# Kernel tuning notes

Measured on AMD Instinct MI355X. Metric: run time of the kernel, lower is better.

Reference implementation:

```python
import jax, jax.numpy as jnp
import numpy as np

N = 100000   # node_count
F = 128      # dim_in (also top-k pool size: k = ceil(F/N * N) = F)
E = 625000   # edges


def setup_inputs() -> dict:
    key = jax.random.key(0)
    ks = jax.random.split(key, 20)
    s = 1.0 / np.sqrt(F)

    def g(i, shape, scale=s):
        return jax.random.normal(ks[i], shape, dtype=jnp.float32) * scale

    inp = {
        "x": jax.random.normal(ks[0], (N, F), dtype=jnp.float32),
        "edge_index": jax.random.randint(ks[1], (2, E), 0, N),
        "edge_weight": jax.random.uniform(ks[2], (E,), dtype=jnp.float32),
    }
    for l in (1, 2):
        b = 3 + 6 * (l - 1)
        inp[f"p{l}"] = g(b, (F,))              # TopKPooling projection vector
        inp[f"w_ih{l}"] = g(b + 1, (3 * F, F))  # GRU input weights (r,z,n)
        inp[f"w_hh{l}"] = g(b + 2, (3 * F, F))  # GRU hidden weights
        inp[f"b_ih{l}"] = g(b + 3, (3 * F,))
        inp[f"b_hh{l}"] = g(b + 4, (3 * F,))
        inp[f"h0{l}"] = g(b + 5, (F, F))        # EvolveGCNH initial_weight
    inp["lin1_w"] = g(15, (2, F))
    inp["lin1_b"] = g(16, (2,), 0.1)
    inp["lin2_w"] = g(17, (1, 2), 0.5)
    inp["lin2_b"] = g(18, (1,), 0.1)
    return inp


def _gru_step(x_t, h, w_ih, w_hh, b_ih, b_hh):
    # single GRU timestep, batch = F rows, hidden = F
    gi = x_t @ w_ih.T + b_ih
    gh = h @ w_hh.T + b_hh
    i_r, i_z, i_n = jnp.split(gi, 3, axis=-1)
    h_r, h_z, h_n = jnp.split(gh, 3, axis=-1)
    r = jax.nn.sigmoid(i_r + h_r)
    z = jax.nn.sigmoid(i_z + h_z)
    n = jnp.tanh(i_n + r * h_n)
    return (1.0 - z) * n + z * h


def _gcn_conv_fixed_w(x, W, edge_index, edge_weight):
    # GCN with externally supplied weight: out = D^-1/2 (A+I) D^-1/2 (x W)
    row, col = edge_index[0], edge_index[1]
    loops = jnp.arange(N)
    row = jnp.concatenate([row, loops])
    col = jnp.concatenate([col, loops])
    w = jnp.concatenate([edge_weight, jnp.ones((N,), x.dtype)])
    deg = jax.ops.segment_sum(w, col, num_segments=N)
    dinv = jnp.where(deg > 0, jax.lax.rsqrt(deg), 0.0)
    norm = dinv[row] * w * dinv[col]          # [E+N]
    xw = x @ W                                 # [N, F]
    return jax.ops.segment_sum(norm[:, None] * xw[row], col, num_segments=N)


def _evolve_gcnh(x, edge_index, edge_weight, p, w_ih, w_hh, b_ih, b_hh, h0):
    # TopKPooling: score = x@p / ||p||, keep top F nodes, gate by tanh(score)
    score = x @ p / jnp.linalg.norm(p)
    top_vals, top_idx = jax.lax.top_k(score, F)
    x_tilde = x[top_idx] * jnp.tanh(top_vals)[:, None]   # [F, F]
    # evolve weight via one GRU step (hidden = previous/initial weight)
    W = _gru_step(x_tilde, h0, w_ih, w_hh, b_ih, b_hh)   # [F, F]
    return _gcn_conv_fixed_w(x, W, edge_index, edge_weight)


def reference(x, edge_index, edge_weight,
              p1, w_ih1, w_hh1, b_ih1, b_hh1, h01,
              p2, w_ih2, w_hh2, b_ih2, b_hh2, h02,
              lin1_w, lin1_b, lin2_w, lin2_b):
    h = jax.nn.relu(_evolve_gcnh(x, edge_index, edge_weight, p1, w_ih1, w_hh1, b_ih1, b_hh1, h01))
    h = jax.nn.relu(_evolve_gcnh(h, edge_index, edge_weight, p2, w_ih2, w_hh2, b_ih2, b_hh2, h02))
    # dropout(0.4) is identity in eval mode
    h = h @ lin1_w.T + lin1_b
    h = h @ lin2_w.T + lin2_b
    return h  # [N, 1]
```

## Files before the change

### kernel.cpp

```cpp
#include <hip/hip_runtime.h>
#include <cstdint>
#include <cstddef>


#define FDIM 128

typedef __attribute__((ext_vector_type(8))) short bfrag;
typedef __attribute__((ext_vector_type(4))) float f32x4;
typedef __attribute__((ext_vector_type(2))) float f32x2;

__device__ __forceinline__ float wave_sum(float v) {
#pragma unroll
  for (int m = 32; m >= 1; m >>= 1) v += __shfl_xor(v, m, 64);
  return v;
}

__device__ __forceinline__ float sigmoidf_(float x) {
  return 1.0f / (1.0f + expf(-x));
}

__device__ __forceinline__ unsigned omap(float f) {
  unsigned u = __float_as_uint(f);
  return (u & 0x80000000u) ? ~u : (u | 0x80000000u);
}

__device__ __forceinline__ int xcd_chunk(int b, int nb) {
  return (b & 7) * (nb >> 3) + (b >> 3);
}

__device__ __forceinline__ int swz(int row, int colb) {
  return row * 256 + (colb ^ ((row & 7) << 4));
}


__global__ void k_edge_deg(const int* __restrict__ ei, const float* __restrict__ ew,
                           float* deg, int* cnt, int E) {
  int e = blockIdx.x * blockDim.x + threadIdx.x;
  if (e < E) {
    int c = ei[E + e];
    atomicAdd(&deg[c], ew[e]);
    atomicAdd(&cnt[c], 1);
  }
}

__global__ void k_scan1(const int* __restrict__ cnt, int* bsum,
                        const float* __restrict__ deg, float* __restrict__ dinv, int n) {
  __shared__ int s[256];
  int b = blockIdx.x, t = threadIdx.x;
  int base = b * 1024;
  int v = 0;
#pragma unroll
  for (int j = 0; j < 4; j++) {
    int i = base + j * 256 + t;
    if (i < n) { v += cnt[i]; dinv[i] = 1.0f / sqrtf(1.0f + deg[i]); }
  }
  s[t] = v; __syncthreads();
  for (int off = 128; off > 0; off >>= 1) { if (t < off) s[t] += s[t + off]; __syncthreads(); }
  if (t == 0) bsum[b] = s[0];
}

__global__ __launch_bounds__(128) void k_scan2_setup(
    int* bsum, int nb, int* rstartN,
    const float* p1, const float* p2, float* invn1, float* invn2,
    const float* l1w, const float* l1b, const float* l2w, const float* l2b,
    float* v, float* cc) {
  __shared__ int s[1024];
  int t = threadIdx.x;
  for (int i = t; i < nb; i += 128) s[i] = bsum[i];
  __syncthreads();
  if (t == 0) {
    int run = 0;
    for (int b = 0; b < nb; b++) { int x = s[b]; s[b] = run; run += x; }
    s[1023] = run;
  }
  __syncthreads();
  for (int i = t; i < nb; i += 128) bsum[i] = s[i];
  if (t == 0) rstartN[0] = s[1023];
  int wv = t >> 6, l = t & 63;
  const float* p = wv ? p2 : p1;
  float2 pv = ((const float2*)p)[l];
  float ss = wave_sum(pv.x * pv.x + pv.y * pv.y);
  if (l == 0) (wv ? invn2 : invn1)[0] = 1.0f / sqrtf(ss);
  v[t] = l2w[0] * l1w[t] + l2w[1] * l1w[128 + t];
  if (t == 0) cc[0] = l2w[0] * l1b[0] + l2w[1] * l1b[1] + l2b[0];
}

__global__ __launch_bounds__(1024) void k_scan3(const int* __restrict__ cnt,
                                                const int* __restrict__ bsum,
                                                int* rstart, int* rnext, int n) {
  __shared__ int s[1024];
  int b = blockIdx.x, t = threadIdx.x;
  int i = b * 1024 + t;
  int v = (i < n) ? cnt[i] : 0;
  s[t] = v; __syncthreads();
  for (int off = 1; off < 1024; off <<= 1) {
    int tmp = (t >= off) ? s[t - off] : 0;
    __syncthreads();
    s[t] += tmp;
    __syncthreads();
  }
  if (i < n) { int ex = bsum[b] + s[t] - v; rstart[i] = ex; rnext[i] = ex; }
}

__global__ void k_fill(const int* __restrict__ ei, const float* __restrict__ ew,
                       const float* __restrict__ dinv, int* rnext, int2* pay, int E) {
  int e = blockIdx.x * blockDim.x + threadIdx.x;
  if (e < E) {
    int r = ei[e];
    int c = ei[E + e];
    float nm = dinv[r] * ew[e] * dinv[c];
    int pos = atomicAdd(&rnext[c], 1);
    pay[pos] = make_int2(r, __float_as_int(nm));
  }
}


__global__ void k_sampdots(const float* __restrict__ x, const float* __restrict__ p,
                           const float* __restrict__ invn, float* __restrict__ samp,
                           int stride) {
  int l = threadIdx.x & 63;
  int w = blockIdx.x * 4 + (threadIdx.x >> 6);
  float2 pv = ((const float2*)p)[l];
  float inv = invn[0];
#pragma unroll
  for (int r = 0; r < 4; r++) {
    int si = w * 4 + r;
    float2 a = ((const float2*)(x + (size_t)(si * stride) * FDIM))[l];
    float s = wave_sum(a.x * pv.x + a.y * pv.y) * inv;
    if (l == 0) samp[si] = s;
  }
}

template <int STRIDED>
__global__ __launch_bounds__(256) void k_thr16(const float* __restrict__ src, int stride,
                                               float* __restrict__ thr) {
  __shared__ float a[2048];
  int t = threadIdx.x;
  for (int i = t; i < 2048; i += 256)
    a[i] = STRIDED ? src[(size_t)i * stride] : src[i];
  __syncthreads();
  int g = blockIdx.x * 256 + t;
  int j = g >> 2, sub = g & 3;
  float v = a[j];
  int gt = 0, eq = 0;
  const float4* a4 = (const float4*)(a + sub * 512);
#pragma unroll 8
  for (int i = 0; i < 128; i++) {
    float4 b = a4[i];
    gt += (b.x > v) + (b.y > v) + (b.z > v) + (b.w > v);
    eq += (b.x == v) + (b.y == v) + (b.z == v) + (b.w == v);
  }
  gt += __shfl_xor(gt, 1, 64); eq += __shfl_xor(eq, 1, 64);
  gt += __shfl_xor(gt, 2, 64); eq += __shfl_xor(eq, 2, 64);
  if (sub == 0 && gt <= 15 && gt + eq > 15) thr[0] = v;
}

__global__ void k_collect(const float* __restrict__ sc, const float* __restrict__ thr,
                          unsigned long long* candk, int* csel, int n) {
  int i = blockIdx.x * blockDim.x + threadIdx.x;
  if (i >= n) return;
  float s = sc[i];
  if (s >= thr[0]) {
    int pos = atomicAdd(csel, 1);
    if (pos < 4096)
      candk[pos] = ((unsigned long long)omap(s) << 32) | (unsigned)(~(unsigned)i);
  }
}

__global__ __launch_bounds__(1024) void k_sel(const unsigned long long* __restrict__ candk,
                                              const int* __restrict__ csel,
                                              int* tidx, float* ttanh) {
  __shared__ unsigned long long a[4104];
  int t = threadIdx.x;
  int nc = csel[0]; if (nc > 4096) nc = 4096;
  int ncp = (nc + 7) & ~7;
  for (int i = t; i < ncp; i += 1024) a[i] = (i < nc) ? candk[i] : 0ULL;
  __syncthreads();
  for (int j = t; j < nc; j += 1024) {
    unsigned long long key = a[j];
    int r = 0;
#pragma unroll 8
    for (int i = 0; i < ncp; i++) r += (a[i] > key);
    if (r < 128) {
      unsigned idx = ~(unsigned)key;
      unsigned hi = (unsigned)(key >> 32);
      unsigned u = (hi & 0x80000000u) ? (hi ^ 0x80000000u) : ~hi;
      tidx[r] = (int)idx;
      ttanh[r] = tanhf(__uint_as_float(u));
    }
  }
}


template <int BF16IN>
__global__ __launch_bounds__(384) void k_gru(const void* __restrict__ xinv,
                                             const int* __restrict__ tidx,
                                             const float* __restrict__ ttanh,
                                             const float* __restrict__ wih,
                                             const float* __restrict__ whh,
                                             const float* __restrict__ bih,
                                             const float* __restrict__ bhh,
                                             const float* __restrict__ h0,
                                             unsigned short* __restrict__ WT_hi,
                                             unsigned short* __restrict__ WT_lo) {
  __shared__ float xt[128], hs[128], gis[384], ghs[384];
  int r = blockIdx.x, t = threadIdx.x;
  if (t < 128) {
    int idx = tidx[r];
    float xv;
    if (BF16IN) {
      unsigned short u = ((const unsigned short*)xinv)[(size_t)idx * FDIM + t];
      xv = __uint_as_float((unsigned)u << 16);
    } else {
      xv = ((const float*)xinv)[(size_t)idx * FDIM + t];
    }
    xt[t] = xv * ttanh[r];
    hs[t] = h0[r * FDIM + t];
  }
  __syncthreads();
  float gi = bih[t], gh = bhh[t];
  const float4* wi4 = (const float4*)(wih + (size_t)t * FDIM);
  const float4* wh4 = (const float4*)(whh + (size_t)t * FDIM);
#pragma unroll 8
  for (int k = 0; k < 32; k++) {
    float4 av = wi4[k], bv = wh4[k];
    gi += av.x * xt[4 * k] + av.y * xt[4 * k + 1] + av.z * xt[4 * k + 2] + av.w * xt[4 * k + 3];
    gh += bv.x * hs[4 * k] + bv.y * hs[4 * k + 1] + bv.z * hs[4 * k + 2] + bv.w * hs[4 * k + 3];
  }
  gis[t] = gi; ghs[t] = gh;
  __syncthreads();
  if (t < 128) {
    float rg = sigmoidf_(gis[t] + ghs[t]);
    float zg = sigmoidf_(gis[t + 128] + ghs[t + 128]);
    float ng = tanhf(gis[t + 256] + rg * ghs[t + 256]);
    float w = (1.0f - zg) * ng + zg * hs[t];
    unsigned u = __float_as_uint(w);
    float res = w - __uint_as_float(u & 0xFFFF0000u);
    WT_hi[t * FDIM + r] = (unsigned short)(u >> 16);
    WT_lo[t * FDIM + r] = (unsigned short)(__float_as_uint(res) >> 16);
  }
}


template <int MODE>
__global__ __launch_bounds__(256) void k_gemm5(const float* __restrict__ Af,
                                               const unsigned short* __restrict__ Ab,
                                               const unsigned short* __restrict__ BTh,
                                               const unsigned short* __restrict__ BTl,
                                               unsigned short* __restrict__ Y2,
                                               float* __restrict__ scOut,
                                               const float* __restrict__ pvec,
                                               const float* __restrict__ invn2,
                                               const float* __restrict__ cc,
                                               int nrows) {
  __shared__ unsigned short sBh[128 * 128];
  __shared__ unsigned short sBl[128 * 128];
  int tid = threadIdx.x;
  int eb = xcd_chunk(blockIdx.x, gridDim.x);
  int rblk = eb * 128;
  if (rblk >= nrows) return;
  for (int i = tid; i < 2048; i += 256) {
    int row = i >> 4, colb = (i & 15) << 4;
    *(uint4*)((char*)sBh + swz(row, colb)) = ((const uint4*)BTh)[i];
    *(uint4*)((char*)sBl + swz(row, colb)) = ((const uint4*)BTl)[i];
  }
  __syncthreads();
  int wv = tid >> 6, l = tid & 63;
  int lcol = l & 15;
  int kgrp = (l >> 4) * 8;

  float pv[8];
#pragma unroll
  for (int ct = 0; ct < 8; ct++) pv[ct] = pvec[ct * 16 + lcol];
  float scale = (MODE == 1) ? invn2[0] : cc[0];

  for (int tile = 0; tile < 2; tile++) {
    int r0 = rblk + wv * 32 + tile * 16;
    if (r0 >= nrows) break;
    int arow = min(r0 + lcol, nrows - 1);
    f32x4 acc[8];
#pragma unroll
    for (int c = 0; c < 8; c++) acc[c] = (f32x4){0.f, 0.f, 0.f, 0.f};
#pragma unroll
    for (int ks = 0; ks < 4; ks++) {
      bfrag ah, al;
      if (MODE == 1) {
        const float* xp = Af + (size_t)arow * FDIM + kgrp + ks * 32;
        float4 v0 = *(const float4*)(xp);
        float4 v1 = *(const float4*)(xp + 4);
        float xs[8] = {v0.x, v0.y, v0.z, v0.w, v1.x, v1.y, v1.z, v1.w};
#pragma unroll
        for (int i = 0; i < 8; i++) {
          unsigned u = __float_as_uint(xs[i]);
          float res = xs[i] - __uint_as_float(u & 0xFFFF0000u);
          ah[i] = (short)(u >> 16);
          al[i] = (short)(__float_as_uint(res) >> 16);
        }
      } else {
        ah = *(const bfrag*)(Ab + (size_t)arow * FDIM + kgrp + ks * 32);
      }
      int colb = (ks * 32 + kgrp) * 2;
#pragma unroll
      for (int ct = 0; ct < 8; ct++) {
        int off = swz(ct * 16 + lcol, colb);
        bfrag bh = *(const bfrag*)((const char*)sBh + off);
        bfrag bl = *(const bfrag*)((const char*)sBl + off);
        acc[ct] = __builtin_amdgcn_mfma_f32_16x16x32_bf16(ah, bh, acc[ct], 0, 0, 0);
        acc[ct] = __builtin_amdgcn_mfma_f32_16x16x32_bf16(ah, bl, acc[ct], 0, 0, 0);
        if (MODE == 1)
          acc[ct] = __builtin_amdgcn_mfma_f32_16x16x32_bf16(al, bh, acc[ct], 0, 0, 0);
      }
    }
    int rbase = r0 + (l >> 4) * 4;
    float part[4] = {0.f, 0.f, 0.f, 0.f};
#pragma unroll
    for (int ct = 0; ct < 8; ct++) {
      int col = ct * 16 + lcol;
#pragma unroll
      for (int r = 0; r < 4; r++) {
        int row = rbase + r;
        float rl = fmaxf(acc[ct][r], 0.0f);
        part[r] += rl * pv[ct];
        if (MODE == 1 && row < nrows) {
          unsigned u = __float_as_uint(rl);
          Y2[(size_t)row * FDIM + col] = (unsigned short)((u + 0x8000u) >> 16);
        }
      }
    }
#pragma unroll
    for (int r = 0; r < 4; r++) {
#pragma unroll
      for (int m = 1; m < 16; m <<= 1) part[r] += __shfl_xor(part[r], m, 64);
    }
    if (lcol == 0) {
#pragma unroll
      for (int r = 0; r < 4; r++) {
        int row = rbase + r;
        if (row < nrows) {
          if (MODE == 1) scOut[row] = part[r] * scale;
          else           scOut[row] = part[r] + scale;
        }
      }
    }
  }
}


template <int L>
__global__ void k_gather5(const void* __restrict__ inv, void* __restrict__ outv,
                          const float* __restrict__ dinv,
                          const int* __restrict__ rstart,
                          const int2* __restrict__ pay,
                          const float* __restrict__ p1, const float* __restrict__ invn1,
                          const float* __restrict__ thr1,
                          unsigned long long* __restrict__ candk, int* __restrict__ csel,
                          int n) {
  int wv = threadIdx.x >> 6, l = threadIdx.x & 63;
  int eb = xcd_chunk(blockIdx.x, gridDim.x);
  int c = eb * 4 + wv;
  if (c >= n) return;
  float dc = dinv[c];
  float ax, ay, sx0, sx1;
  unsigned long long base;
  if (L == 1) {
    const float* in = (const float*)inv;
    float2 v = ((const float2*)(in + (size_t)c * FDIM))[l];
    sx0 = v.x; sx1 = v.y;
    ax = dc * dc * v.x; ay = dc * dc * v.y;
    base = (unsigned long long)(const char*)inv + ((size_t)l << 3);
  } else {
    const unsigned short* in = (const unsigned short*)inv;
    unsigned u = *(const unsigned*)(in + (size_t)c * FDIM + l * 2);
    sx0 = sx1 = 0.f;
    ax = dc * dc * __uint_as_float(u << 16);
    ay = dc * dc * __uint_as_float(u & 0xFFFF0000u);
    base = (unsigned long long)(const char*)inv + ((size_t)l << 2);
  }
  int st = rstart[c], cn = rstart[c + 1] - st;
  for (int q0 = 0; q0 < cn; q0 += 64) {
    int2 ep = (q0 + l < cn) ? pay[st + q0 + l] : make_int2(c, 0);
    int m = min(64, cn - q0);
    for (int g = 0; g < m; g += 8) {
      unsigned long long addr[8];
      float w[8];
#pragma unroll
      for (int u = 0; u < 8; u++) {
        int r = __shfl(ep.x, g + u, 64);
        w[u] = __int_as_float(__shfl(ep.y, g + u, 64));
        addr[u] = base + ((unsigned long long)(unsigned)r << (L == 1 ? 9 : 8));
      }
      if (L == 1) {
        f32x2 ev[8];
#pragma unroll
        for (int u = 0; u < 8; u++)
          asm volatile("global_load_dwordx2 %0, %1, off" : "=v"(ev[u]) : "v"(addr[u]));
        asm volatile("s_waitcnt vmcnt(0)" ::: "memory");
        __builtin_amdgcn_sched_barrier(0);
#pragma unroll
        for (int u = 0; u < 8; u++) { ax += w[u] * ev[u][0]; ay += w[u] * ev[u][1]; }
      } else {
        unsigned uv[8];
#pragma unroll
        for (int u = 0; u < 8; u++)
          asm volatile("global_load_dword %0, %1, off" : "=v"(uv[u]) : "v"(addr[u]));
        asm volatile("s_waitcnt vmcnt(0)" ::: "memory");
        __builtin_amdgcn_sched_barrier(0);
#pragma unroll
        for (int u = 0; u < 8; u++) {
          ax += w[u] * __uint_as_float(uv[u] << 16);
          ay += w[u] * __uint_as_float(uv[u] & 0xFFFF0000u);
        }
      }
    }
  }
  if (L == 1) {
    float* out = (float*)outv;
    ((float2*)(out + (size_t)c * FDIM))[l] = make_float2(ax, ay);
    float2 pvv = ((const float2*)p1)[l];
    float s = wave_sum(sx0 * pvv.x + sx1 * pvv.y) * invn1[0];
    if (l == 0 && s >= thr1[0]) {
      int pos = atomicAdd(csel, 1);
      if (pos < 4096)
        candk[pos] = ((unsigned long long)omap(s) << 32) | (unsigned)(~(unsigned)c);
    }
  } else {
    unsigned* out = (unsigned*)outv;
    unsigned lo = (__float_as_uint(ax) + 0x8000u) >> 16;
    unsigned hi = (__float_as_uint(ay) + 0x8000u) >> 16;
    out[(size_t)c * (FDIM / 2) + l] = lo | (hi << 16);
  }
}


extern "C" void kernel_launch(void* const* d_in, const int* in_sizes, int n_in,
                              void* d_out, int out_size, void* d_ws, size_t ws_size,
                              hipStream_t stream) {
  const float* x    = (const float*)d_in[0];
  const int*   ei   = (const int*)d_in[1];
  const float* ew   = (const float*)d_in[2];
  const float* p1   = (const float*)d_in[3];
  const float* wih1 = (const float*)d_in[4];
  const float* whh1 = (const float*)d_in[5];
  const float* bih1 = (const float*)d_in[6];
  const float* bhh1 = (const float*)d_in[7];
  const float* h01  = (const float*)d_in[8];
  const float* p2   = (const float*)d_in[9];
  const float* wih2 = (const float*)d_in[10];
  const float* whh2 = (const float*)d_in[11];
  const float* bih2 = (const float*)d_in[12];
  const float* bhh2 = (const float*)d_in[13];
  const float* h02  = (const float*)d_in[14];
  const float* l1w  = (const float*)d_in[15];
  const float* l1b  = (const float*)d_in[16];
  const float* l2w  = (const float*)d_in[17];
  const float* l2b  = (const float*)d_in[18];
  float* out = (float*)d_out;

  const int N = in_sizes[0] / FDIM;
  const int E = in_sizes[2];

  size_t off = 0;
  auto alloc = [&](size_t bytes) -> char* {
    char* p = (char*)d_ws + off;
    off = (off + bytes + 255) & ~(size_t)255;
    return p;
  };
  float* deg   = (float*)alloc((size_t)N * 4);
  int*   cnt   = (int*)alloc((size_t)N * 4);
  int*   csel1 = (int*)alloc(8);
  int*   csel2 = (int*)alloc(8);
  size_t zero_span = (size_t)((char*)(csel2 + 2) - (char*)deg);
  float* sc2   = (float*)alloc((size_t)N * 4);
  unsigned long long* candk = (unsigned long long*)alloc(4096 * 8);
  int*   tidx  = (int*)alloc(128 * 4);
  float* ttanh = (float*)alloc(128 * 4);
  float* invn1 = (float*)alloc(4);
  float* invn2 = (float*)alloc(4);
  float* thr1  = (float*)alloc(4);
  float* thr2  = (float*)alloc(4);
  float* samp  = (float*)alloc(2048 * 4);
  float* dinv  = (float*)alloc((size_t)N * 4);
  int*   rstart= (int*)alloc((size_t)(N + 1) * 4);
  int*   rnext = (int*)alloc((size_t)N * 4);
  const int nb = (N + 1023) / 1024;
  int*   bsum  = (int*)alloc((size_t)nb * 4);
  int2*  pay   = (int2*)alloc((size_t)E * 8);
  float* vvec  = (float*)alloc(128 * 4);
  float* cc    = (float*)alloc(4);
  unsigned short* WTh = (unsigned short*)alloc(128 * 128 * 2);
  unsigned short* WTl = (unsigned short*)alloc(128 * 128 * 2);
  float* g1    = (float*)alloc((size_t)N * FDIM * 4);
  unsigned short* h1 = (unsigned short*)alloc((size_t)N * FDIM * 2);
  unsigned short* g2 = (unsigned short*)alloc((size_t)N * FDIM * 2);
  (void)ws_size; (void)n_in; (void)out_size;

  const int gemmblocks   = ((N + 127) / 128 + 7) & ~7;
  const int gatherblocks = (N + 3) / 4;
  const int sampstride   = N / 2048;

  hipMemsetAsync(deg, 0, zero_span, stream);
  k_edge_deg<<<(E + 255) / 256, 256, 0, stream>>>(ei, ew, deg, cnt, E);
  k_scan1<<<nb, 256, 0, stream>>>(cnt, bsum, deg, dinv, N);
  k_scan2_setup<<<1, 128, 0, stream>>>(bsum, nb, rstart + N, p1, p2, invn1, invn2,
                                       l1w, l1b, l2w, l2b, vvec, cc);
  k_scan3<<<nb, 1024, 0, stream>>>(cnt, bsum, rstart, rnext, N);
  k_fill<<<(E + 255) / 256, 256, 0, stream>>>(ei, ew, dinv, rnext, pay, E);

  k_sampdots<<<128, 256, 0, stream>>>(x, p1, invn1, samp, sampstride);
  k_thr16<0><<<32, 256, 0, stream>>>(samp, 1, thr1);
  k_gather5<1><<<gatherblocks, 256, 0, stream>>>(x, g1, dinv, rstart, pay,
                                                 p1, invn1, thr1, candk, csel1, N);
  k_sel<<<1, 1024, 0, stream>>>(candk, csel1, tidx, ttanh);
  k_gru<0><<<128, 384, 0, stream>>>(x, tidx, ttanh, wih1, whh1, bih1, bhh1, h01, WTh, WTl);
  k_gemm5<1><<<gemmblocks, 256, 0, stream>>>(g1, nullptr, WTh, WTl, h1, sc2,
                                             p2, invn2, cc, N);

  k_thr16<1><<<32, 256, 0, stream>>>(sc2, sampstride, thr2);
  k_collect<<<(N + 255) / 256, 256, 0, stream>>>(sc2, thr2, candk, csel2, N);
  k_sel<<<1, 1024, 0, stream>>>(candk, csel2, tidx, ttanh);
  k_gru<1><<<128, 384, 0, stream>>>(h1, tidx, ttanh, wih2, whh2, bih2, bhh2, h02, WTh, WTl);
  k_gather5<2><<<gatherblocks, 256, 0, stream>>>(h1, g2, dinv, rstart, pay,
                                                 nullptr, nullptr, nullptr, nullptr, nullptr, N);
  k_gemm5<2><<<gemmblocks, 256, 0, stream>>>(nullptr, g2, WTh, WTl, nullptr, out,
                                             vvec, nullptr, cc, N);
}
```

Measured before the change: 323.0 us.

## Fuse neighbor gather with dense GEMM epilogue via LDS staging

Merges the sparse aggregation kernel and the following MFMA GEMM into one kernel. Each wave gathers 16 aggregated rows into shared memory, then feeds them straight into the bf16 split MFMA. This removes the N×128 intermediate g1/g2 buffers and their write and read-back traffic. Layer-1 top-k scoring, which used to ride along in the gather, moves into a separate k_scorecollect pass that must now run before the GRU. The B operand is read from global or L1 each time rather than from swizzled LDS, and each block covers fewer rows, which may cost some GEMM efficiency.

```diff
diff --git a/kernel.cpp b/kernel.cpp
--- a/kernel.cpp
+++ b/kernel.cpp
@@ -26,10 +26,6 @@
 
 __device__ __forceinline__ int xcd_chunk(int b, int nb) {
   return (b & 7) * (nb >> 3) + (b >> 3);
-}
-
-__device__ __forceinline__ int swz(int row, int colb) {
-  return row * 256 + (colb ^ ((row & 7) << 4));
 }
 
 
@@ -153,6 +149,28 @@
   gt += __shfl_xor(gt, 1, 64); eq += __shfl_xor(eq, 1, 64);
   gt += __shfl_xor(gt, 2, 64); eq += __shfl_xor(eq, 2, 64);
   if (sub == 0 && gt <= 15 && gt + eq > 15) thr[0] = v;
+}
+
+__global__ void k_scorecollect(const float* __restrict__ x, const float* __restrict__ p,
+                               const float* __restrict__ invn, const float* __restrict__ thr,
+                               unsigned long long* __restrict__ candk, int* __restrict__ csel,
+                               int n) {
+  int l = threadIdx.x & 63;
+  int eb = xcd_chunk(blockIdx.x, gridDim.x);
+  int base = (eb * 4 + (threadIdx.x >> 6)) * 16;
+  if (base >= n) return;
+  float2 pv = ((const float2*)p)[l];
+  float inv = invn[0], th = thr[0];
+  int lim = min(16, n - base);
+  for (int r = 0; r < lim; r++) {
+    float2 a = ((const float2*)(x + (size_t)(base + r) * FDIM))[l];
+    float s = wave_sum(a.x * pv.x + a.y * pv.y) * inv;
+    if (l == 0 && s >= th) {
+      int pos = atomicAdd(csel, 1);
+      if (pos < 4096)
+        candk[pos] = ((unsigned long long)omap(s) << 32) | (unsigned)(~(unsigned)(base + r));
+    }
+  }
 }
 
 __global__ void k_collect(const float* __restrict__ sc, const float* __restrict__ thr,
@@ -243,191 +261,154 @@
 
 
 template <int MODE>
-__global__ __launch_bounds__(256) void k_gemm5(const float* __restrict__ Af,
-                                               const unsigned short* __restrict__ Ab,
-                                               const unsigned short* __restrict__ BTh,
-                                               const unsigned short* __restrict__ BTl,
-                                               unsigned short* __restrict__ Y2,
-                                               float* __restrict__ scOut,
-                                               const float* __restrict__ pvec,
-                                               const float* __restrict__ invn2,
-                                               const float* __restrict__ cc,
-                                               int nrows) {
-  __shared__ unsigned short sBh[128 * 128];
-  __shared__ unsigned short sBl[128 * 128];
+__global__ __launch_bounds__(256) void k_fgg(const void* __restrict__ inv,
+                                             const unsigned short* __restrict__ BTh,
+                                             const unsigned short* __restrict__ BTl,
+                                             const float* __restrict__ dinv,
+                                             const int* __restrict__ rstart,
+                                             const int2* __restrict__ pay,
+                                             unsigned short* __restrict__ Y2,
+                                             float* __restrict__ scOut,
+                                             const float* __restrict__ pvec,
+                                             const float* __restrict__ scal,
+                                             int n) {
+  __shared__ float gst[4][16][132];
   int tid = threadIdx.x;
+  int wv = tid >> 6, l = tid & 63;
   int eb = xcd_chunk(blockIdx.x, gridDim.x);
-  int rblk = eb * 128;
-  if (rblk >= nrows) return;
-  for (int i = tid; i < 2048; i += 256) {
-    int row = i >> 4, colb = (i & 15) << 4;
-    *(uint4*)((char*)sBh + swz(row, colb)) = ((const uint4*)BTh)[i];
-    *(uint4*)((char*)sBl + swz(row, colb)) = ((const uint4*)BTl)[i];
-  }
-  __syncthreads();
-  int wv = tid >> 6, l = tid & 63;
-  int lcol = l & 15;
-  int kgrp = (l >> 4) * 8;
-
-  float pv[8];
-#pragma unroll
-  for (int ct = 0; ct < 8; ct++) pv[ct] = pvec[ct * 16 + lcol];
-  float scale = (MODE == 1) ? invn2[0] : cc[0];
-
-  for (int tile = 0; tile < 2; tile++) {
-    int r0 = rblk + wv * 32 + tile * 16;
-    if (r0 >= nrows) break;
-    int arow = min(r0 + lcol, nrows - 1);
-    f32x4 acc[8];
-#pragma unroll
-    for (int c = 0; c < 8; c++) acc[c] = (f32x4){0.f, 0.f, 0.f, 0.f};
-#pragma unroll
-    for (int ks = 0; ks < 4; ks++) {
-      bfrag ah, al;
+  int base = eb * 64 + wv * 16;
+
+  for (int i = 0; i < 16; i++) {
+    int c = base + i;
+    float ax = 0.f, ay = 0.f;
+    if (c < n) {
+      float dc = dinv[c];
+      unsigned long long rb;
       if (MODE == 1) {
-        const float* xp = Af + (size_t)arow * FDIM + kgrp + ks * 32;
-        float4 v0 = *(const float4*)(xp);
-        float4 v1 = *(const float4*)(xp + 4);
-        float xs[8] = {v0.x, v0.y, v0.z, v0.w, v1.x, v1.y, v1.z, v1.w};
-#pragma unroll
-        for (int i = 0; i < 8; i++) {
-          unsigned u = __float_as_uint(xs[i]);
-          float res = xs[i] - __uint_as_float(u & 0xFFFF0000u);
-          ah[i] = (short)(u >> 16);
-          al[i] = (short)(__float_as_uint(res) >> 16);
-        }
+        const float* in = (const float*)inv;
+        float2 v = ((const float2*)(in + (size_t)c * FDIM))[l];
+        ax = dc * dc * v.x; ay = dc * dc * v.y;
+        rb = (unsigned long long)(const char*)inv + ((size_t)l << 3);
       } else {
-        ah = *(const bfrag*)(Ab + (size_t)arow * FDIM + kgrp + ks * 32);
+        const unsigned short* in = (const unsigned short*)inv;
+        unsigned u = *(const unsigned*)(in + (size_t)c * FDIM + l * 2);
+        ax = dc * dc * __uint_as_float(u << 16);
+        ay = dc * dc * __uint_as_float(u & 0xFFFF0000u);
+        rb = (unsigned long long)(const char*)inv + ((size_t)l << 2);
       }
-      int colb = (ks * 32 + kgrp) * 2;
-#pragma unroll
-      for (int ct = 0; ct < 8; ct++) {
-        int off = swz(ct * 16 + lcol, colb);
-        bfrag bh = *(const bfrag*)((const char*)sBh + off);
-        bfrag bl = *(const bfrag*)((const char*)sBl + off);
-        acc[ct] = __builtin_amdgcn_mfma_f32_16x16x32_bf16(ah, bh, acc[ct], 0, 0, 0);
-        acc[ct] = __builtin_amdgcn_mfma_f32_16x16x32_bf16(ah, bl, acc[ct], 0, 0, 0);
-        if (MODE == 1)
-          acc[ct] = __builtin_amdgcn_mfma_f32_16x16x32_bf16(al, bh, acc[ct], 0, 0, 0);
-      }
-    }
-    int rbase = r0 + (l >> 4) * 4;
-    float part[4] = {0.f, 0.f, 0.f, 0.f};
-#pragma unroll
-    for (int ct = 0; ct < 8; ct++) {
-      int col = ct * 16 + lcol;
-#pragma unroll
-      for (int r = 0; r < 4; r++) {
-        int row = rbase + r;
-        float rl = fmaxf(acc[ct][r], 0.0f);
-        part[r] += rl * pv[ct];
-        if (MODE == 1 && row < nrows) {
-          unsigned u = __float_as_uint(rl);
-          Y2[(size_t)row * FDIM + col] = (unsigned short)((u + 0x8000u) >> 16);
+      int st = rstart[c], cn = rstart[c + 1] - st;
+      for (int q0 = 0; q0 < cn; q0 += 64) {
+        int2 ep = (q0 + l < cn) ? pay[st + q0 + l] : make_int2(c, 0);
+        int m = min(64, cn - q0);
+        for (int g = 0; g < m; g += 8) {
+          unsigned long long addr[8];
+          float w[8];
+#pragma unroll
+          for (int u = 0; u < 8; u++) {
+            int r = __shfl(ep.x, g + u, 64);
+            w[u] = __int_as_float(__shfl(ep.y, g + u, 64));
+            addr[u] = rb + ((unsigned long long)(unsigned)r << (MODE == 1 ? 9 : 8));
+          }
+          if (MODE == 1) {
+            f32x2 ev[8];
+#pragma unroll
+            for (int u = 0; u < 8; u++)
+              asm volatile("global_load_dwordx2 %0, %1, off" : "=v"(ev[u]) : "v"(addr[u]));
+            asm volatile("s_waitcnt vmcnt(0)" ::: "memory");
+            __builtin_amdgcn_sched_barrier(0);
+#pragma unroll
+            for (int u = 0; u < 8; u++) { ax += w[u] * ev[u][0]; ay += w[u] * ev[u][1]; }
+          } else {
+            unsigned uv[8];
+#pragma unroll
+            for (int u = 0; u < 8; u++)
+              asm volatile("global_load_dword %0, %1, off" : "=v"(uv[u]) : "v"(addr[u]));
+            asm volatile("s_waitcnt vmcnt(0)" ::: "memory");
+            __builtin_amdgcn_sched_barrier(0);
+#pragma unroll
+            for (int u = 0; u < 8; u++) {
+              ax += w[u] * __uint_as_float(uv[u] << 16);
+              ay += w[u] * __uint_as_float(uv[u] & 0xFFFF0000u);
+            }
+          }
         }
       }
     }
+    if (MODE == 2) {
+      ax = __uint_as_float((__float_as_uint(ax) + 0x8000u) & 0xFFFF0000u);
+      ay = __uint_as_float((__float_as_uint(ay) + 0x8000u) & 0xFFFF0000u);
+    }
+    gst[wv][i][2 * l]     = ax;
+    gst[wv][i][2 * l + 1] = ay;
+  }
+
+  int lcol = l & 15, q = l >> 4;
+  float pv[8];
+#pragma unroll
+  for (int ct = 0; ct < 8; ct++) pv[ct] = pvec[ct * 16 + lcol];
+  float scale = scal[0];
+
+  f32x4 acc[8];
+#pragma unroll
+  for (int c = 0; c < 8; c++) acc[c] = (f32x4){0.f, 0.f, 0.f, 0.f};
+
+#pragma unroll
+  for (int ks = 0; ks < 4; ks++) {
+    const f32x4* gp = (const f32x4*)&gst[wv][lcol][q * 8 + ks * 32];
+    f32x4 v0 = gp[0], v1 = gp[1];
+    float xs[8] = {v0[0], v0[1], v0[2], v0[3], v1[0], v1[1], v1[2], v1[3]};
+    bfrag ah, al;
+#pragma unroll
+    for (int i = 0; i < 8; i++) {
+      unsigned u = __float_as_uint(xs[i]);
+      ah[i] = (short)(u >> 16);
+      if (MODE == 1) {
+        float res = xs[i] - __uint_as_float(u & 0xFFFF0000u);
+        al[i] = (short)(__float_as_uint(res) >> 16);
+      }
+    }
+#pragma unroll
+    for (int ct = 0; ct < 8; ct++) {
+      size_t boff = (size_t)(ct * 16 + lcol) * FDIM + ks * 32 + q * 8;
+      bfrag bh = *(const bfrag*)(BTh + boff);
+      bfrag bl = *(const bfrag*)(BTl + boff);
+      acc[ct] = __builtin_amdgcn_mfma_f32_16x16x32_bf16(ah, bh, acc[ct], 0, 0, 0);
+      acc[ct] = __builtin_amdgcn_mfma_f32_16x16x32_bf16(ah, bl, acc[ct], 0, 0, 0);
+      if (MODE == 1)
+        acc[ct] = __builtin_amdgcn_mfma_f32_16x16x32_bf16(al, bh, acc[ct], 0, 0, 0);
+    }
+  }
+
+  int rbase = base + q * 4;
+  float part[4] = {0.f, 0.f, 0.f, 0.f};
+#pragma unroll
+  for (int ct = 0; ct < 8; ct++) {
+    int col = ct * 16 + lcol;
 #pragma unroll
     for (int r = 0; r < 4; r++) {
-#pragma unroll
-      for (int m = 1; m < 16; m <<= 1) part[r] += __shfl_xor(part[r], m, 64);
-    }
-    if (lcol == 0) {
-#pragma unroll
-      for (int r = 0; r < 4; r++) {
-        int row = rbase + r;
-        if (row < nrows) {
-          if (MODE == 1) scOut[row] = part[r] * scale;
-          else           scOut[row] = part[r] + scale;
-        }
+      int row = rbase + r;
+      float rl = fmaxf(acc[ct][r], 0.0f);
+      part[r] += rl * pv[ct];
+      if (MODE == 1 && row < n) {
+        unsigned u = __float_as_uint(rl);
+        Y2[(size_t)row * FDIM + col] = (unsigned short)((u + 0x8000u) >> 16);
       }
     }
   }
-}
-
-
-template <int L>
-__global__ void k_gather5(const void* __restrict__ inv, void* __restrict__ outv,
-                          const float* __restrict__ dinv,
-                          const int* __restrict__ rstart,
-                          const int2* __restrict__ pay,
-                          const float* __restrict__ p1, const float* __restrict__ invn1,
-                          const float* __restrict__ thr1,
-                          unsigned long long* __restrict__ candk, int* __restrict__ csel,
-                          int n) {
-  int wv = threadIdx.x >> 6, l = threadIdx.x & 63;
-  int eb = xcd_chunk(blockIdx.x, gridDim.x);
-  int c = eb * 4 + wv;
-  if (c >= n) return;
-  float dc = dinv[c];
-  float ax, ay, sx0, sx1;
-  unsigned long long base;
-  if (L == 1) {
-    const float* in = (const float*)inv;
-    float2 v = ((const float2*)(in + (size_t)c * FDIM))[l];
-    sx0 = v.x; sx1 = v.y;
-    ax = dc * dc * v.x; ay = dc * dc * v.y;
-    base = (unsigned long long)(const char*)inv + ((size_t)l << 3);
-  } else {
-    const unsigned short* in = (const unsigned short*)inv;
-    unsigned u = *(const unsigned*)(in + (size_t)c * FDIM + l * 2);
-    sx0 = sx1 = 0.f;
-    ax = dc * dc * __uint_as_float(u << 16);
-    ay = dc * dc * __uint_as_float(u & 0xFFFF0000u);
-    base = (unsigned long long)(const char*)inv + ((size_t)l << 2);
-  }
-  int st = rstart[c], cn = rstart[c + 1] - st;
-  for (int q0 = 0; q0 < cn; q0 += 64) {
-    int2 ep = (q0 + l < cn) ? pay[st + q0 + l] : make_int2(c, 0);
-    int m = min(64, cn - q0);
-    for (int g = 0; g < m; g += 8) {
-      unsigned long long addr[8];
-      float w[8];
-#pragma unroll
-      for (int u = 0; u < 8; u++) {
-        int r = __shfl(ep.x, g + u, 64);
-        w[u] = __int_as_float(__shfl(ep.y, g + u, 64));
-        addr[u] = base + ((unsigned long long)(unsigned)r << (L == 1 ? 9 : 8));
+#pragma unroll
+  for (int r = 0; r < 4; r++) {
+#pragma unroll
+    for (int m = 1; m < 16; m <<= 1) part[r] += __shfl_xor(part[r], m, 64);
+  }
+  if (lcol == 0) {
+#pragma unroll
+    for (int r = 0; r < 4; r++) {
+      int row = rbase + r;
+      if (row < n) {
+        if (MODE == 1) scOut[row] = part[r] * scale;
+        else           scOut[row] = part[r] + scale;
       }
-      if (L == 1) {
-        f32x2 ev[8];
-#pragma unroll
-        for (int u = 0; u < 8; u++)
-          asm volatile("global_load_dwordx2 %0, %1, off" : "=v"(ev[u]) : "v"(addr[u]));
-        asm volatile("s_waitcnt vmcnt(0)" ::: "memory");
-        __builtin_amdgcn_sched_barrier(0);
-#pragma unroll
-        for (int u = 0; u < 8; u++) { ax += w[u] * ev[u][0]; ay += w[u] * ev[u][1]; }
-      } else {
-        unsigned uv[8];
-#pragma unroll
-        for (int u = 0; u < 8; u++)
-          asm volatile("global_load_dword %0, %1, off" : "=v"(uv[u]) : "v"(addr[u]));
-        asm volatile("s_waitcnt vmcnt(0)" ::: "memory");
-        __builtin_amdgcn_sched_barrier(0);
-#pragma unroll
-        for (int u = 0; u < 8; u++) {
-          ax += w[u] * __uint_as_float(uv[u] << 16);
-          ay += w[u] * __uint_as_float(uv[u] & 0xFFFF0000u);
-        }
-      }
-    }
-  }
-  if (L == 1) {
-    float* out = (float*)outv;
-    ((float2*)(out + (size_t)c * FDIM))[l] = make_float2(ax, ay);
-    float2 pvv = ((const float2*)p1)[l];
-    float s = wave_sum(sx0 * pvv.x + sx1 * pvv.y) * invn1[0];
-    if (l == 0 && s >= thr1[0]) {
-      int pos = atomicAdd(csel, 1);
-      if (pos < 4096)
-        candk[pos] = ((unsigned long long)omap(s) << 32) | (unsigned)(~(unsigned)c);
-    }
-  } else {
-    unsigned* out = (unsigned*)outv;
-    unsigned lo = (__float_as_uint(ax) + 0x8000u) >> 16;
-    unsigned hi = (__float_as_uint(ay) + 0x8000u) >> 16;
-    out[(size_t)c * (FDIM / 2) + l] = lo | (hi << 16);
+    }
   }
 }
 
@@ -489,14 +470,12 @@
   float* cc    = (float*)alloc(4);
   unsigned short* WTh = (unsigned short*)alloc(128 * 128 * 2);
   unsigned short* WTl = (unsigned short*)alloc(128 * 128 * 2);
-  float* g1    = (float*)alloc((size_t)N * FDIM * 4);
   unsigned short* h1 = (unsigned short*)alloc((size_t)N * FDIM * 2);
-  unsigned short* g2 = (unsigned short*)alloc((size_t)N * FDIM * 2);
   (void)ws_size; (void)n_in; (void)out_size;
 
-  const int gemmblocks   = ((N + 127) / 128 + 7) & ~7;
-  const int gatherblocks = (N + 3) / 4;
-  const int sampstride   = N / 2048;
+  const int scoreblocks = (((N + 15) / 16 + 3) / 4 + 7) & ~7;
+  const int fggblocks   = ((N + 63) / 64 + 7) & ~7;
+  const int sampstride  = N / 2048;
 
   hipMemsetAsync(deg, 0, zero_span, stream);
   k_edge_deg<<<(E + 255) / 256, 256, 0, stream>>>(ei, ew, deg, cnt, E);
@@ -508,19 +487,16 @@
 
   k_sampdots<<<128, 256, 0, stream>>>(x, p1, invn1, samp, sampstride);
   k_thr16<0><<<32, 256, 0, stream>>>(samp, 1, thr1);
-  k_gather5<1><<<gatherblocks, 256, 0, stream>>>(x, g1, dinv, rstart, pay,
-                                                 p1, invn1, thr1, candk, csel1, N);
+  k_scorecollect<<<scoreblocks, 256, 0, stream>>>(x, p1, invn1, thr1, candk, csel1, N);
   k_sel<<<1, 1024, 0, stream>>>(candk, csel1, tidx, ttanh);
   k_gru<0><<<128, 384, 0, stream>>>(x, tidx, ttanh, wih1, whh1, bih1, bhh1, h01, WTh, WTl);
-  k_gemm5<1><<<gemmblocks, 256, 0, stream>>>(g1, nullptr, WTh, WTl, h1, sc2,
-                                             p2, invn2, cc, N);
+  k_fgg<1><<<fggblocks, 256, 0, stream>>>(x, WTh, WTl, dinv, rstart, pay,
+                                          h1, sc2, p2, invn2, N);
 
   k_thr16<1><<<32, 256, 0, stream>>>(sc2, sampstride, thr2);
   k_collect<<<(N + 255) / 256, 256, 0, stream>>>(sc2, thr2, candk, csel2, N);
   k_sel<<<1, 1024, 0, stream>>>(candk, csel2, tidx, ttanh);
   k_gru<1><<<128, 384, 0, stream>>>(h1, tidx, ttanh, wih2, whh2, bih2, bhh2, h02, WTh, WTl);
-  k_gather5<2><<<gatherblocks, 256, 0, stream>>>(h1, g2, dinv, rstart, pay,
-                                                 nullptr, nullptr, nullptr, nullptr, nullptr, N);
-  k_gemm5<2><<<gemmblocks, 256, 0, stream>>>(nullptr, g2, WTh, WTl, nullptr, out,
-                                             vvec, nullptr, cc, N);
-}
+  k_fgg<2><<<fggblocks, 256, 0, stream>>>(h1, WTh, WTl, dinv, rstart, pay,
+                                          nullptr, out, vvec, cc, N);
+}
```

Result: slower. 433.2 us (+34.1%).
